# Optimization experiments

Hardware: AMD Instinct MI355X
Metric: run time of the kernel (lower is better)

## Reference

```python
import jax, jax.numpy as jnp
import numpy as np

TWO_PI = 2.0 * np.pi
P = 3      # AR order
KMAX = 5   # winding offsets per side
D = 3      # torus dimension

def setup_inputs() -> dict:
    key = jax.random.key(0)
    kg, kphi = jax.random.split(key)
    g = jax.random.normal(kg, (32, 16, 2048, D), dtype=jnp.float32)  # (n_mc, n_samples, T, d) angles
    ar_phi = 0.1 * jax.random.normal(kphi, (D, P), dtype=jnp.float32)
    ar_eta = 0.05 * jnp.ones((D,), dtype=jnp.float32)
    ar_c = jnp.zeros((D,), dtype=jnp.float32)
    return {"g": g, "ar_phi": ar_phi, "ar_eta": ar_eta, "ar_c": ar_c}

def _logmap(x):
    # Torus logmap: wrap to (-pi, pi]
    return jnp.mod(x + np.pi, TWO_PI) - np.pi

def reference(g, ar_phi, ar_eta, ar_c):
    # prms: (ar_c, ar_phi, ar_eta**2); scale = sqrt(eta)
    scale = jnp.sqrt(jnp.square(ar_eta))  # (d,) == |ar_eta|
    # Torus: inverse(g) = -g, gmul = add
    dg = g[..., 1:, :] - g[..., :-1, :]
    dx = _logmap(dg)                       # (..., T-1, d)
    Td = dx.shape[-2]
    # AR history stack: (..., T', d, p), T' = T-1-p
    hist = jnp.stack([dx[..., P - j - 1:Td - j - 1, :] for j in range(P)], axis=-1)
    dy = dx[..., P:, :] - (ar_phi * hist).sum(-1)  # (..., T', d)
    ks = jnp.arange(-KMAX, KMAX + 1, dtype=dy.dtype)
    z = dy[..., :, None] + TWO_PI * ks             # (..., T', d, K)
    log_scale = jnp.log(scale)
    lp = (-0.5 * jnp.square((z - ar_c[:, None]) / scale[:, None])
          - log_scale[:, None]
          - 0.5 * jnp.log(jnp.asarray(TWO_PI, dy.dtype)))
    # Faithful to the diagonal branch of ARP.forward: per-dim log_q with d=1
    # logsumexp's over a size-1 axis (identity) then .sum(-1) over the K
    # winding offsets, i.e. the winding log-probs are SUMMED (not logsumexp'd),
    # then summed over dims j.
    lq = lp.sum(-1).sum(-1)                # (..., T')
    return lq.sum(-1).sum(-1)              # (n_mc,)
```

## Files before the change

### kernel.cpp

```cpp
#include <hip/hip_runtime.h>
#include <math.h>

#define T 2048
#define D 3
#define P 3
#define NK 11
#define SUM_K2 110.0f
#define TWO_PI_F 6.28318530717958647692f
#define INV_TWO_PI_F 0.15915494309189533577f
#define PI_F 3.14159265358979323846f

__device__ __forceinline__ float wrap_pi(float x) {
    float k = rintf(x * INV_TWO_PI_F);
    return fmaf(-k, TWO_PI_F, x);
}

__global__ __launch_bounds__(256) void arp_kernel(
    const float* __restrict__ g,
    const float* __restrict__ ar_phi,
    const float* __restrict__ ar_eta,
    const float* __restrict__ ar_c,
    float* __restrict__ out,
    int n_samples)
{
    __shared__ float sg[T * D];
    __shared__ float sdx[(T - 1) * D];
    __shared__ float wave_sums[4];

    const int series = blockIdx.x;
    const int mc     = series / n_samples;
    const int tid    = threadIdx.x;

    {
        const float4* src = (const float4*)(g + (size_t)series * (T * D));
        float4* dst = (float4*)sg;
        const int nvec = (T * D) / 4;
        for (int i = tid; i < nvec; i += 256) dst[i] = src[i];
    }
    __syncthreads();

    {
        const int n = (T - 1) * D;
        for (int i = tid; i < n; i += 256) sdx[i] = wrap_pi(sg[i + D] - sg[i]);
    }
    __syncthreads();

    float ph[D][P], inv_s2[D], cc[D];
    float Cd_sum = 0.0f;
    #pragma unroll
    for (int d = 0; d < D; ++d) {
        float s = fabsf(ar_eta[d]);
        inv_s2[d] = 1.0f / (s * s);
        cc[d] = ar_c[d];
        #pragma unroll
        for (int j = 0; j < P; ++j) ph[d][j] = ar_phi[d * P + j];
        Cd_sum += -0.5f * inv_s2[d] * (4.0f * PI_F * PI_F * SUM_K2)
                  - (float)NK * logf(s)
                  - 0.5f * (float)NK * logf(TWO_PI_F);
    }

    const int Tp = T - 1 - P;
    float acc = 0.0f;
    for (int t = tid; t < Tp; t += 256) {
        float w[12];
        #pragma unroll
        for (int m = 0; m < 12; ++m) w[m] = sdx[t * D + m];
        #pragma unroll
        for (int d = 0; d < D; ++d) {
            float dy = w[9 + d] - (ph[d][0] * w[6 + d]
                                 + ph[d][1] * w[3 + d]
                                 + ph[d][2] * w[d]);
            float z = dy - cc[d];
            acc += -0.5f * (float)NK * z * z * inv_s2[d];
        }
    }

    #pragma unroll
    for (int off = 32; off > 0; off >>= 1) acc += __shfl_down(acc, off, 64);
    const int wave = tid >> 6, lane = tid & 63;
    if (lane == 0) wave_sums[wave] = acc;
    __syncthreads();
    if (tid == 0) {
        float block_sum = wave_sums[0] + wave_sums[1] + wave_sums[2] + wave_sums[3];
        block_sum += (float)Tp * Cd_sum;
        atomicAdd(&out[mc], block_sum);
    }
}

extern "C" void kernel_launch(void* const* d_in, const int* in_sizes, int n_in,
                              void* d_out, int out_size, void* d_ws, size_t ws_size,
                              hipStream_t stream) {
    const float* g      = (const float*)d_in[0];
    const float* ar_phi = (const float*)d_in[1];
    const float* ar_eta = (const float*)d_in[2];
    const float* ar_c   = (const float*)d_in[3];
    float* out = (float*)d_out;

    const int n_series  = in_sizes[0] / (T * D);
    const int n_mc      = out_size;
    const int n_samples = n_series / n_mc;

    hipMemsetAsync(out, 0, (size_t)out_size * sizeof(float), stream);
    arp_kernel<<<n_series, 256, 0, stream>>>(g, ar_phi, ar_eta, ar_c, out, n_samples);
}
```

Before: 72.36 us.

## Split each time series across four blocks with halo loads

Each series is now handled by four blocks, each covering 511 output timesteps plus a small halo of input samples. The grid grows from 512 to 2048 blocks and shared memory per block shrinks, which should raise occupancy and let more loads be in flight on a memory-bound kernel. The cost is about four times as many atomic adds into the output and some redundant halo loads.

After: 87.77 us. 21.3% more time.

```diff
diff --git a/kernel.cpp b/kernel.cpp
--- a/kernel.cpp
+++ b/kernel.cpp
@@ -9,6 +9,9 @@
 #define TWO_PI_F 6.28318530717958647692f
 #define INV_TWO_PI_F 0.15915494309189533577f
 #define PI_F 3.14159265358979323846f
+
+#define SPLIT 4
+#define SEG 511
 
 __device__ __forceinline__ float wrap_pi(float x) {
     float k = rintf(x * INV_TWO_PI_F);
@@ -23,25 +26,33 @@
     float* __restrict__ out,
     int n_samples)
 {
-    __shared__ float sg[T * D];
-    __shared__ float sdx[(T - 1) * D];
+    __shared__ float sg[SEG * 3 + 12 + 4];
+    __shared__ float sdx[(SEG + 3) * 3];
     __shared__ float wave_sums[4];
 
-    const int series = blockIdx.x;
-    const int mc     = series / n_samples;
+    const int blk    = blockIdx.x;
+    const int series = blk >> 2;
+    const int seg    = blk & (SPLIT - 1);
     const int tid    = threadIdx.x;
 
+    const int t0      = seg * SEG;
+    const int start_f = t0 * 3;
+    const int a0      = start_f & ~3;
+    const int ofs     = start_f - a0;
+    const int nfloat  = SEG * 3 + 12 + ofs;
+    const int nvec    = (nfloat + 3) >> 2;
+
     {
-        const float4* src = (const float4*)(g + (size_t)series * (T * D));
+        const float4* src = (const float4*)(g + (size_t)series * (T * D) + a0);
         float4* dst = (float4*)sg;
-        const int nvec = (T * D) / 4;
         for (int i = tid; i < nvec; i += 256) dst[i] = src[i];
     }
     __syncthreads();
 
     {
-        const int n = (T - 1) * D;
-        for (int i = tid; i < n; i += 256) sdx[i] = wrap_pi(sg[i + D] - sg[i]);
+        const int n = (SEG + 3) * 3;
+        for (int f = tid; f < n; f += 256)
+            sdx[f] = wrap_pi(sg[ofs + f + 3] - sg[ofs + f]);
     }
     __syncthreads();
 
@@ -59,12 +70,11 @@
                   - 0.5f * (float)NK * logf(TWO_PI_F);
     }
 
-    const int Tp = T - 1 - P;
     float acc = 0.0f;
-    for (int t = tid; t < Tp; t += 256) {
+    for (int t = tid; t < SEG; t += 256) {
         float w[12];
         #pragma unroll
-        for (int m = 0; m < 12; ++m) w[m] = sdx[t * D + m];
+        for (int m = 0; m < 12; ++m) w[m] = sdx[t * 3 + m];
         #pragma unroll
         for (int d = 0; d < D; ++d) {
             float dy = w[9 + d] - (ph[d][0] * w[6 + d]
@@ -82,7 +92,8 @@
     __syncthreads();
     if (tid == 0) {
         float block_sum = wave_sums[0] + wave_sums[1] + wave_sums[2] + wave_sums[3];
-        block_sum += (float)Tp * Cd_sum;
+        block_sum += (float)SEG * Cd_sum;
+        const int mc = series / n_samples;
         atomicAdd(&out[mc], block_sum);
     }
 }
@@ -101,5 +112,5 @@
     const int n_samples = n_series / n_mc;
 
     hipMemsetAsync(out, 0, (size_t)out_size * sizeof(float), stream);
-    arp_kernel<<<n_series, 256, 0, stream>>>(g, ar_phi, ar_eta, ar_c, out, n_samples);
+    arp_kernel<<<n_series * SPLIT, 256, 0, stream>>>(g, ar_phi, ar_eta, ar_c, out, n_samples);
 }
```
